# Kernel tuning notes

Measured on AMD Instinct MI355X. Metric: run time of the kernel, lower is better.

The kernel has to match this reference:

```python
import jax, jax.numpy as jnp
import numpy as np

N_NODES = 50000
N_EDGES = 600000
IN_DIM = 128
HID_DIM = 256
LAT_DIM = 64


def setup_inputs() -> dict:
    key = jax.random.key(0)
    k_x, k_e, k_w1, k_b1, k_w2, k_b2 = jax.random.split(key, 6)
    x = jax.random.normal(k_x, (N_NODES, IN_DIM), dtype=jnp.float32)
    edge_index = jax.random.randint(k_e, (2, N_EDGES), 0, N_NODES, dtype=jnp.int64)
    # torch nn.Linear default init: U(-1/sqrt(fan_in), 1/sqrt(fan_in))
    lim1 = 1.0 / np.sqrt(2 * IN_DIM)
    lim2 = 1.0 / np.sqrt(HID_DIM)
    W1 = jax.random.uniform(k_w1, (2 * IN_DIM, HID_DIM), jnp.float32, -lim1, lim1)
    b1 = jax.random.uniform(k_b1, (HID_DIM,), jnp.float32, -lim1, lim1)
    W2 = jax.random.uniform(k_w2, (HID_DIM, LAT_DIM), jnp.float32, -lim2, lim2)
    b2 = jax.random.uniform(k_b2, (LAT_DIM,), jnp.float32, -lim2, lim2)
    return {"x": x, "edge_index": edge_index, "W1": W1, "b1": b1, "W2": W2, "b2": b2}


def reference(x, edge_index, W1, b1, W2, b2):
    h_i = x[edge_index[0]]                     # [E, D]
    h_j = x[edge_index[1]]                     # [E, D]
    edge_features = jnp.concatenate([h_i, h_j], axis=-1)  # [E, 2D]
    hidden = jax.nn.relu(edge_features @ W1 + b1)          # [E, H]
    return hidden @ W2 + b2                                # [E, L]
```

## Files before the change

### kernel.cpp

```cpp
#include <hip/hip_runtime.h>

#define E_TOTAL 600000
#define N_NODES 50000
#define ETILE 96
#define NETILES 6250
#define NNT 391
#define LDH2 136
#define LDH3 264

typedef __attribute__((ext_vector_type(8))) short short8;
typedef __attribute__((ext_vector_type(8))) _Float16 half8;
typedef __attribute__((ext_vector_type(4))) float f32x4;

__device__ __forceinline__ unsigned f2bf_u(float f) {
  union { float f; unsigned u; } v; v.f = f;
  return (v.u + 0x7fffu + ((v.u >> 16) & 1u)) >> 16;
}
__device__ __forceinline__ unsigned short f2h_u(float f) {
  union { _Float16 h; unsigned short u; } v; v.h = (_Float16)f;
  return v.u;
}

__global__ __launch_bounds__(256) void prep(
    const float* __restrict__ W1, const float* __restrict__ W2,
    const float* __restrict__ b1,
    unsigned short* __restrict__ W1c, unsigned short* __restrict__ W2t2,
    unsigned short* __restrict__ b1h) {
  __shared__ float t[32][33];
  int bid = blockIdx.x;
  int tx = threadIdx.x & 31, ty = threadIdx.x >> 5;
  if (bid < 64) {
    int k0 = (bid >> 3) * 32, n0 = (bid & 7) * 32;
#pragma unroll
    for (int i = 0; i < 32; i += 8) t[ty + i][tx] = W1[(k0 + ty + i) * 256 + n0 + tx];
    __syncthreads();
    int coff = (k0 >= 128) ? 256 : 0;
#pragma unroll
    for (int i = 0; i < 32; i += 8)
      W1c[(n0 + ty + i + coff) * 128 + (k0 & 127) + tx] = (unsigned short)f2bf_u(t[tx][ty + i]);
  } else if (bid < 80) {
    int b = bid - 64;
    int k0 = (b >> 1) * 32, n0 = (b & 1) * 32;
#pragma unroll
    for (int i = 0; i < 32; i += 8) t[ty + i][tx] = W2[(k0 + ty + i) * 64 + n0 + tx];
    __syncthreads();
#pragma unroll
    for (int i = 0; i < 32; i += 8)
      W2t2[(n0 + ty + i) * 256 + k0 + tx] = f2h_u(t[tx][ty + i]);
  } else {
    b1h[threadIdx.x] = f2h_u(b1[threadIdx.x]);
  }
}

__global__ __launch_bounds__(256, 2) void node_uv(
    const float* __restrict__ x, const unsigned short* __restrict__ W1c,
    unsigned short* __restrict__ UV) {
  __shared__ __align__(16) unsigned short xt[128 * LDH2];
  const int tid = threadIdx.x;
  const int bid = blockIdx.x;
  const int ntile = bid >> 1, chalf = bid & 1;
  const int n0 = ntile * 128;
  const int lane = tid & 63, w = tid >> 6, m = lane & 15, q = lane >> 4;

  const int kb = (tid & 15) * 8;
  const int e0 = tid >> 4;
#pragma unroll
  for (int i = 0; i < 8; ++i) {
    int r = e0 + 16 * i;
    int n = n0 + r; if (n >= N_NODES) n = N_NODES - 1;
    const float* p = x + n * 128 + kb;
    f32x4 g0 = *(const f32x4*)p, g1 = *(const f32x4*)(p + 4);
    short8 s;
#pragma unroll
    for (int j = 0; j < 4; ++j) { s[j] = (short)f2bf_u(g0[j]); s[4 + j] = (short)f2bf_u(g1[j]); }
    *(short8*)&xt[r * LDH2 + kb] = s;
  }

  int w1o[4];
#pragma unroll
  for (int nt = 0; nt < 4; ++nt) w1o[nt] = (chalf * 256 + (w * 4 + nt) * 16 + m) * 128 + q * 8;
  short8 wa[2][4];
#pragma unroll
  for (int nt = 0; nt < 4; ++nt) wa[0][nt] = *(const short8*)&W1c[w1o[nt]];

  __syncthreads();

  f32x4 acc[4][8];
#pragma unroll
  for (int nt = 0; nt < 4; ++nt)
#pragma unroll
    for (int mt = 0; mt < 8; ++mt) acc[nt][mt] = (f32x4){0.f, 0.f, 0.f, 0.f};

#pragma unroll
  for (int kk = 0; kk < 4; ++kk) {
    const int cur = kk & 1, nx = cur ^ 1;
    if (kk < 3) {
#pragma unroll
      for (int nt = 0; nt < 4; ++nt) wa[nx][nt] = *(const short8*)&W1c[w1o[nt] + (kk + 1) * 32];
    }
    short8 f[8];
#pragma unroll
    for (int mt = 0; mt < 8; ++mt)
      f[mt] = *(const short8*)&xt[(mt * 16 + m) * LDH2 + kk * 32 + q * 8];
#pragma unroll
    for (int nt = 0; nt < 4; ++nt)
#pragma unroll
      for (int mt = 0; mt < 8; ++mt)
        acc[nt][mt] = __builtin_amdgcn_mfma_f32_16x16x32_bf16(wa[cur][nt], f[mt], acc[nt][mt], 0, 0, 0);
  }

#pragma unroll
  for (int nt = 0; nt < 4; ++nt)
#pragma unroll
    for (int mt = 0; mt < 8; ++mt) {
      int n = n0 + mt * 16 + m;
      if (n < N_NODES) {
        union { _Float16 h[4]; uint2 u; } pk;
#pragma unroll
        for (int r = 0; r < 4; ++r) pk.h[r] = (_Float16)acc[nt][mt][r];
        *(uint2*)&UV[n * 512 + chalf * 256 + w * 64 + nt * 16 + q * 4] = pk.u;
      }
    }
}

__global__ __launch_bounds__(256, 2) void edge_mlp(
    const unsigned short* __restrict__ UV, const int* __restrict__ ei,
    const unsigned short* __restrict__ W2t2, const unsigned short* __restrict__ b1h,
    const float* __restrict__ b2, float* __restrict__ out) {
  __shared__ __align__(16) unsigned short hid[ETILE * LDH3];
  const int tid = threadIdx.x;
  const int base = blockIdx.x * ETILE;
  const int lane = tid & 63, w = tid >> 6, m = lane & 15, q = lane >> 4;
  const int c = tid & 31;
  const int e0 = tid >> 5;

  half8 w2r[8];
  const int w2off = (w * 16 + m) * 256 + q * 8;
#pragma unroll
  for (int kk = 0; kk < 8; ++kk) w2r[kk] = *(const half8*)&W2t2[w2off + kk * 32];
  half8 bias = *(const half8*)&b1h[c * 8];
  f32x4 b2v = *(const f32x4*)&b2[w * 16 + q * 4];

  int si[12], di[12];
#pragma unroll
  for (int i = 0; i < 12; ++i) {
    int e = base + e0 + 8 * i;
    si[i] = ei[e];
    di[i] = ei[E_TOTAL + e];
  }

#pragma unroll
  for (int g = 0; g < 2; ++g) {
    half8 lu[6], lv[6];
#pragma unroll
    for (int i = 0; i < 6; ++i) {
      const int r = g * 6 + i;
      lu[i] = *(const half8*)&UV[(size_t)si[r] * 512 + c * 8];
      lv[i] = *(const half8*)&UV[(size_t)di[r] * 512 + 256 + c * 8];
    }
#pragma unroll
    for (int i = 0; i < 6; ++i) {
      const int r = g * 6 + i;
      half8 s = lu[i] + lv[i] + bias;
#pragma unroll
      for (int j = 0; j < 8; ++j) s[j] = s[j] > (_Float16)0 ? s[j] : (_Float16)0;
      *(half8*)&hid[(e0 + 8 * r) * LDH3 + c * 8] = s;
    }
  }

  __syncthreads();

  f32x4 acc2[6];
#pragma unroll
  for (int mt = 0; mt < 6; ++mt) acc2[mt] = (f32x4){0.f, 0.f, 0.f, 0.f};
#pragma unroll
  for (int kk = 0; kk < 8; ++kk) {
#pragma unroll
    for (int mt = 0; mt < 6; ++mt) {
      half8 h = *(const half8*)&hid[(mt * 16 + m) * LDH3 + kk * 32 + q * 8];
      acc2[mt] = __builtin_amdgcn_mfma_f32_16x16x32_f16(w2r[kk], h, acc2[mt], 0, 0, 0);
    }
  }

#pragma unroll
  for (int mt = 0; mt < 6; ++mt) {
    f32x4 o;
#pragma unroll
    for (int r = 0; r < 4; ++r) o[r] = acc2[mt][r] + b2v[r];
    __builtin_nontemporal_store(o, (f32x4*)&out[(size_t)(base + mt * 16 + m) * 64 + w * 16 + q * 4]);
  }
}

extern "C" void kernel_launch(void* const* d_in, const int* in_sizes, int n_in,
                              void* d_out, int out_size, void* d_ws, size_t ws_size,
                              hipStream_t stream) {
  const float* x  = (const float*)d_in[0];
  const int*   ei = (const int*)d_in[1];
  const float* W1 = (const float*)d_in[2];
  const float* b1 = (const float*)d_in[3];
  const float* W2 = (const float*)d_in[4];
  const float* b2 = (const float*)d_in[5];
  float* out = (float*)d_out;

  unsigned short* W1c  = (unsigned short*)d_ws;
  unsigned short* W2t2 = W1c + 512 * 128;
  unsigned short* b1h  = W2t2 + 64 * 256;
  unsigned short* UV   = b1h + 256;

  prep<<<81, 256, 0, stream>>>(W1, W2, b1, W1c, W2t2, b1h);
  node_uv<<<NNT * 2, 256, 0, stream>>>(x, W1c, UV);
  edge_mlp<<<NETILES, 256, 0, stream>>>(UV, ei, W2t2, b1h, b2, out);
}
```

Measured before the change: 304.9 us.

## Shrink node and edge tiles to 64 rows and stage UV stores through LDS

```diff
diff --git a/kernel.cpp b/kernel.cpp
--- a/kernel.cpp
+++ b/kernel.cpp
@@ -2,11 +2,10 @@
 
 #define E_TOTAL 600000
 #define N_NODES 50000
-#define ETILE 96
-#define NETILES 6250
-#define NNT 391
-#define LDH2 136
-#define LDH3 264
+#define NETILES 9375
+#define NNT 782
+#define LDS_X 136
+#define LDP 264
 
 typedef __attribute__((ext_vector_type(8))) short short8;
 typedef __attribute__((ext_vector_type(8))) _Float16 half8;
@@ -52,28 +51,27 @@
   }
 }
 
-__global__ __launch_bounds__(256, 2) void node_uv(
+__global__ __launch_bounds__(256, 3) void node_uv(
     const float* __restrict__ x, const unsigned short* __restrict__ W1c,
     unsigned short* __restrict__ UV) {
-  __shared__ __align__(16) unsigned short xt[128 * LDH2];
+  __shared__ __align__(16) unsigned short xt[64 * LDP];
   const int tid = threadIdx.x;
-  const int bid = blockIdx.x;
-  const int ntile = bid >> 1, chalf = bid & 1;
-  const int n0 = ntile * 128;
+  const int ntile = (int)blockIdx.x >> 1, chalf = blockIdx.x & 1;
+  const int n0 = ntile * 64;
   const int lane = tid & 63, w = tid >> 6, m = lane & 15, q = lane >> 4;
 
   const int kb = (tid & 15) * 8;
-  const int e0 = tid >> 4;
-#pragma unroll
-  for (int i = 0; i < 8; ++i) {
-    int r = e0 + 16 * i;
+  const int r0 = tid >> 4;
+#pragma unroll
+  for (int i = 0; i < 4; ++i) {
+    int r = r0 + 16 * i;
     int n = n0 + r; if (n >= N_NODES) n = N_NODES - 1;
-    const float* p = x + n * 128 + kb;
+    const float* p = x + (size_t)n * 128 + kb;
     f32x4 g0 = *(const f32x4*)p, g1 = *(const f32x4*)(p + 4);
     short8 s;
 #pragma unroll
     for (int j = 0; j < 4; ++j) { s[j] = (short)f2bf_u(g0[j]); s[4 + j] = (short)f2bf_u(g1[j]); }
-    *(short8*)&xt[r * LDH2 + kb] = s;
+    *(short8*)&xt[r * LDS_X + kb] = s;
   }
 
   int w1o[4];
@@ -85,11 +83,11 @@
 
   __syncthreads();
 
-  f32x4 acc[4][8];
+  f32x4 acc[4][4];
 #pragma unroll
   for (int nt = 0; nt < 4; ++nt)
 #pragma unroll
-    for (int mt = 0; mt < 8; ++mt) acc[nt][mt] = (f32x4){0.f, 0.f, 0.f, 0.f};
+    for (int mt = 0; mt < 4; ++mt) acc[nt][mt] = (f32x4){0.f, 0.f, 0.f, 0.f};
 
 #pragma unroll
   for (int kk = 0; kk < 4; ++kk) {
@@ -98,38 +96,49 @@
 #pragma unroll
       for (int nt = 0; nt < 4; ++nt) wa[nx][nt] = *(const short8*)&W1c[w1o[nt] + (kk + 1) * 32];
     }
-    short8 f[8];
-#pragma unroll
-    for (int mt = 0; mt < 8; ++mt)
-      f[mt] = *(const short8*)&xt[(mt * 16 + m) * LDH2 + kk * 32 + q * 8];
+    short8 f[4];
+#pragma unroll
+    for (int mt = 0; mt < 4; ++mt)
+      f[mt] = *(const short8*)&xt[(mt * 16 + m) * LDS_X + kk * 32 + q * 8];
 #pragma unroll
     for (int nt = 0; nt < 4; ++nt)
 #pragma unroll
-      for (int mt = 0; mt < 8; ++mt)
+      for (int mt = 0; mt < 4; ++mt)
         acc[nt][mt] = __builtin_amdgcn_mfma_f32_16x16x32_bf16(wa[cur][nt], f[mt], acc[nt][mt], 0, 0, 0);
   }
 
+  __syncthreads();
+
 #pragma unroll
   for (int nt = 0; nt < 4; ++nt)
 #pragma unroll
-    for (int mt = 0; mt < 8; ++mt) {
-      int n = n0 + mt * 16 + m;
-      if (n < N_NODES) {
-        union { _Float16 h[4]; uint2 u; } pk;
-#pragma unroll
-        for (int r = 0; r < 4; ++r) pk.h[r] = (_Float16)acc[nt][mt][r];
-        *(uint2*)&UV[n * 512 + chalf * 256 + w * 64 + nt * 16 + q * 4] = pk.u;
-      }
-    }
-}
-
-__global__ __launch_bounds__(256, 2) void edge_mlp(
+    for (int mt = 0; mt < 4; ++mt) {
+      union { _Float16 h[4]; uint2 u; } pk;
+#pragma unroll
+      for (int r = 0; r < 4; ++r) pk.h[r] = (_Float16)acc[nt][mt][r];
+      *(uint2*)&xt[(mt * 16 + m) * LDP + (w * 4 + nt) * 16 + q * 4] = pk.u;
+    }
+
+  __syncthreads();
+
+  const int rr = tid >> 2, c8 = tid & 3;
+  if (n0 + rr < N_NODES) {
+    unsigned short* dst = UV + (size_t)(n0 + rr) * 512 + chalf * 256;
+#pragma unroll
+    for (int i = 0; i < 8; ++i) {
+      int ch = c8 + 4 * i;
+      *(short8*)&dst[ch * 8] = *(const short8*)&xt[rr * LDP + ch * 8];
+    }
+  }
+}
+
+__global__ __launch_bounds__(256, 4) void edge_mlp(
     const unsigned short* __restrict__ UV, const int* __restrict__ ei,
     const unsigned short* __restrict__ W2t2, const unsigned short* __restrict__ b1h,
     const float* __restrict__ b2, float* __restrict__ out) {
-  __shared__ __align__(16) unsigned short hid[ETILE * LDH3];
+  __shared__ __align__(16) unsigned short hid[64 * LDP];
   const int tid = threadIdx.x;
-  const int base = blockIdx.x * ETILE;
+  const int base = blockIdx.x * 64;
   const int lane = tid & 63, w = tid >> 6, m = lane & 15, q = lane >> 4;
   const int c = tid & 31;
   const int e0 = tid >> 5;
@@ -141,9 +150,9 @@
   half8 bias = *(const half8*)&b1h[c * 8];
   f32x4 b2v = *(const f32x4*)&b2[w * 16 + q * 4];
 
-  int si[12], di[12];
-#pragma unroll
-  for (int i = 0; i < 12; ++i) {
+  int si[8], di[8];
+#pragma unroll
+  for (int i = 0; i < 8; ++i) {
     int e = base + e0 + 8 * i;
     si[i] = ei[e];
     di[i] = ei[E_TOTAL + e];
@@ -151,39 +160,39 @@
 
 #pragma unroll
   for (int g = 0; g < 2; ++g) {
-    half8 lu[6], lv[6];
-#pragma unroll
-    for (int i = 0; i < 6; ++i) {
-      const int r = g * 6 + i;
+    half8 lu[4], lv[4];
+#pragma unroll
+    for (int i = 0; i < 4; ++i) {
+      const int r = g * 4 + i;
       lu[i] = *(const half8*)&UV[(size_t)si[r] * 512 + c * 8];
       lv[i] = *(const half8*)&UV[(size_t)di[r] * 512 + 256 + c * 8];
     }
 #pragma unroll
-    for (int i = 0; i < 6; ++i) {
-      const int r = g * 6 + i;
+    for (int i = 0; i < 4; ++i) {
+      const int r = g * 4 + i;
       half8 s = lu[i] + lv[i] + bias;
 #pragma unroll
       for (int j = 0; j < 8; ++j) s[j] = s[j] > (_Float16)0 ? s[j] : (_Float16)0;
-      *(half8*)&hid[(e0 + 8 * r) * LDH3 + c * 8] = s;
-    }
-  }
-
-  __syncthreads();
-
-  f32x4 acc2[6];
-#pragma unroll
-  for (int mt = 0; mt < 6; ++mt) acc2[mt] = (f32x4){0.f, 0.f, 0.f, 0.f};
+      *(half8*)&hid[(e0 + 8 * r) * LDP + c * 8] = s;
+    }
+  }
+
+  __syncthreads();
+
+  f32x4 acc2[4];
+#pragma unroll
+  for (int mt = 0; mt < 4; ++mt) acc2[mt] = (f32x4){0.f, 0.f, 0.f, 0.f};
 #pragma unroll
   for (int kk = 0; kk < 8; ++kk) {
 #pragma unroll
-    for (int mt = 0; mt < 6; ++mt) {
-      half8 h = *(const half8*)&hid[(mt * 16 + m) * LDH3 + kk * 32 + q * 8];
+    for (int mt = 0; mt < 4; ++mt) {
+      half8 h = *(const half8*)&hid[(mt * 16 + m) * LDP + kk * 32 + q * 8];
       acc2[mt] = __builtin_amdgcn_mfma_f32_16x16x32_f16(w2r[kk], h, acc2[mt], 0, 0, 0);
     }
   }
 
 #pragma unroll
-  for (int mt = 0; mt < 6; ++mt) {
+  for (int mt = 0; mt < 4; ++mt) {
     f32x4 o;
 #pragma unroll
     for (int r = 0; r < 4; ++r) o[r] = acc2[mt][r] + b2v[r];
```

Measured after the change: 290.9 us. -4.6%, faster.
